# Kernel optimization log

Measured on AMD Instinct MI355X. Metric: run time of the kernel, lower is better.

## Reference

```python
import jax, jax.numpy as jnp
import numpy as np

N_NODES = 40000
N_EDGES = 640000
IN_DIM = 128
HID_DIM = 256
OUT_DIM = 256
N_CLASSES = 10
N_GRAPHS = 128
NEG_SLOPE = 0.01  # F.leaky_relu default


def setup_inputs() -> dict:
    key = jax.random.key(0)
    ks = jax.random.split(key, 10)
    x = jax.random.normal(ks[0], (N_NODES, IN_DIM), dtype=jnp.float32)
    src = jax.random.randint(ks[1], (N_EDGES,), 0, N_NODES, dtype=jnp.int64)
    dst = jax.random.randint(ks[2], (N_EDGES,), 0, N_NODES, dtype=jnp.int64)
    graph_ids = jnp.sort(jax.random.randint(ks[3], (N_NODES,), 0, N_GRAPHS, dtype=jnp.int64))
    # GraphConv weights (glorot-ish scale) and biases
    W1 = jax.random.normal(ks[4], (IN_DIM, HID_DIM), dtype=jnp.float32) * (1.0 / np.sqrt(IN_DIM))
    b1 = jnp.zeros((HID_DIM,), dtype=jnp.float32)
    W2 = jax.random.normal(ks[5], (HID_DIM, OUT_DIM), dtype=jnp.float32) * (1.0 / np.sqrt(HID_DIM))
    b2 = jnp.zeros((OUT_DIM,), dtype=jnp.float32)
    Wc = jax.random.normal(ks[6], (OUT_DIM, N_CLASSES), dtype=jnp.float32) * (1.0 / np.sqrt(OUT_DIM))
    bc = jnp.zeros((N_CLASSES,), dtype=jnp.float32)
    return {"x": x, "src": src, "dst": dst, "graph_ids": graph_ids,
            "W1": W1, "b1": b1, "W2": W2, "b2": b2, "Wc": Wc, "bc": bc}


def reference(x, src, dst, graph_ids, W1, b1, W2, b2, Wc, bc):
    n = x.shape[0]
    ones_e = jnp.ones((src.shape[0],), dtype=x.dtype)
    # degrees (clamped at 1, as DGL GraphConv does)
    outdeg = jnp.clip(jax.ops.segment_sum(ones_e, src, num_segments=n), 1.0)
    indeg = jnp.clip(jax.ops.segment_sum(ones_e, dst, num_segments=n), 1.0)
    inv_sqrt_out = jax.lax.rsqrt(outdeg)[:, None]   # [N,1]
    inv_sqrt_in = jax.lax.rsqrt(indeg)[:, None]     # [N,1]

    def gconv(h, W, b):
        # DGL GraphConv, norm='both': D_in^{-1/2} A D_out^{-1/2} h W + b
        m = h * inv_sqrt_out                                    # [N,d]
        agg = jnp.zeros((n, h.shape[1]), h.dtype).at[dst].add(m[src])
        agg = agg * inv_sqrt_in
        return agg @ W + b

    h = jax.nn.leaky_relu(gconv(x, W1, b1), negative_slope=NEG_SLOPE)
    h = jax.nn.leaky_relu(gconv(h, W2, b2), negative_slope=NEG_SLOPE)

    # dgl.mean_nodes: per-graph mean over nodes
    sums = jax.ops.segment_sum(h, graph_ids, num_segments=N_GRAPHS)        # [G,256]
    counts = jax.ops.segment_sum(jnp.ones((n,), h.dtype), graph_ids, num_segments=N_GRAPHS)
    hg = sums / jnp.clip(counts, 1.0)[:, None]
    return hg @ Wc + bc  # [G, n_classes]
```

## Files before the change

kernel.cpp:

```cpp
#include <hip/hip_runtime.h>

#define N_NODES 40000
#define N_EDGES 640000
#define IN_DIM 128
#define HID_DIM 256
#define OUT_DIM 256
#define N_CLASSES 10
#define N_GRAPHS 128
#define NEG_SLOPE 0.01f

#define SCAN_BLOCKS ((N_NODES + 255) / 256)

typedef short bf16x8 __attribute__((ext_vector_type(8)));
typedef float f32x4 __attribute__((ext_vector_type(4)));

__device__ inline unsigned short f2bf(float x) {
  unsigned u = __float_as_uint(x);
  u += 0x7fffu + ((u >> 16) & 1u);
  return (unsigned short)(u >> 16);
}
__device__ inline float bf2f(unsigned short h) {
  return __uint_as_float(((unsigned)h) << 16);
}
__device__ inline unsigned pack_split(float v) {
  unsigned short hi = f2bf(v);
  float r = v - bf2f(hi);
  unsigned short lo = f2bf(r);
  return (unsigned)hi | ((unsigned)lo << 16);
}

__global__ __launch_bounds__(256) void hist_kernel(const int* __restrict__ src,
                                                   const int* __restrict__ dst,
                                                   int* __restrict__ cntOut,
                                                   int* __restrict__ cntIn, int nEdges) {
  int i = blockIdx.x * 256 + threadIdx.x;
  if (i < nEdges) {
    atomicAdd(&cntOut[src[i]], 1);
    atomicAdd(&cntIn[dst[i]], 1);
  }
}

__global__ __launch_bounds__(256) void scan1_kernel(const int* __restrict__ cnt,
                                                    int* __restrict__ rowptr,
                                                    int* __restrict__ blockSums) {
  __shared__ int sm[256];
  int i = blockIdx.x * 256 + threadIdx.x;
  int v = (i < N_NODES) ? cnt[i] : 0;
  sm[threadIdx.x] = v;
  __syncthreads();
  for (int off = 1; off < 256; off <<= 1) {
    int t = (threadIdx.x >= off) ? sm[threadIdx.x - off] : 0;
    __syncthreads();
    sm[threadIdx.x] += t;
    __syncthreads();
  }
  if (i < N_NODES) rowptr[i] = sm[threadIdx.x] - v;
  if (threadIdx.x == 255) blockSums[blockIdx.x] = sm[255];
}

__global__ __launch_bounds__(256) void scan2_kernel(const int* __restrict__ blockSums,
                                                    int* __restrict__ blockOff,
                                                    int* __restrict__ rowptr) {
  __shared__ int sm[256];
  int tid = threadIdx.x;
  int v = (tid < SCAN_BLOCKS) ? blockSums[tid] : 0;
  sm[tid] = v;
  __syncthreads();
  for (int off = 1; off < 256; off <<= 1) {
    int t = (tid >= off) ? sm[tid - off] : 0;
    __syncthreads();
    sm[tid] += t;
    __syncthreads();
  }
  if (tid < SCAN_BLOCKS) blockOff[tid] = sm[tid] - v;
  if (tid == 255) rowptr[N_NODES] = sm[255];
}

__global__ __launch_bounds__(256) void scan3_kernel(int* __restrict__ rowptr,
                                                    const int* __restrict__ blockOff,
                                                    int* __restrict__ cursor,
                                                    const int* __restrict__ cntIn,
                                                    const int* __restrict__ cntOut,
                                                    float* __restrict__ sIn,
                                                    float* __restrict__ sOut,
                                                    float* __restrict__ poolZero, int nZero) {
  int i = blockIdx.x * 256 + threadIdx.x;
  if (i < N_NODES) {
    int r = rowptr[i] + blockOff[blockIdx.x];
    rowptr[i] = r;
    cursor[i] = r;
    sIn[i] = rsqrtf((float)max(cntIn[i], 1));
    sOut[i] = rsqrtf((float)max(cntOut[i], 1));
  }
  if (i < nZero) poolZero[i] = 0.0f;
}

__global__ __launch_bounds__(256) void fill_kernel(const int* __restrict__ src,
                                                   const int* __restrict__ dst,
                                                   int* __restrict__ cursor,
                                                   int* __restrict__ eidx, int nEdges) {
  int e = blockIdx.x * 256 + threadIdx.x;
  if (e < nEdges) {
    int pos = atomicAdd(&cursor[dst[e]], 1);
    eidx[pos] = src[e];
  }
}

__global__ __launch_bounds__(256) void wsplit_kernel(const float* __restrict__ W1,
                                                     unsigned* __restrict__ Wt1,
                                                     const float* __restrict__ W2,
                                                     unsigned* __restrict__ Wt2) {
  int i = blockIdx.x * 256 + threadIdx.x;
  constexpr int N1 = IN_DIM * 256;
  if (i < N1) {
    int k = i >> 8;
    int n = i & 255;
    Wt1[(size_t)n * IN_DIM + k] = pack_split(W1[i]);
  } else {
    int j = i - N1;
    if (j < HID_DIM * 256) {
      int k = j >> 8;
      int n = j & 255;
      Wt2[(size_t)n * HID_DIM + k] = pack_split(W2[j]);
    }
  }
}

template <int D, bool BF16>
__global__ __launch_bounds__(256) void gather_kernel(const void* __restrict__ hsrc,
                                                     const float* __restrict__ s_out,
                                                     const float* __restrict__ s_in,
                                                     const int* __restrict__ rowptr,
                                                     const int* __restrict__ eidx,
                                                     unsigned* __restrict__ aggp) {
  constexpr int VEC = D / 64;
  const int node = __builtin_amdgcn_readfirstlane(blockIdx.x * 4 + (threadIdx.x >> 6));
  const int lane = threadIdx.x & 63;
  const int f0 = lane * VEC;
  const int beg = rowptr[node];
  const int end = rowptr[node + 1];
  float acc[VEC] = {};
  int j = beg;
  for (; j + 7 < end; j += 8) {
    int s[8];
#pragma unroll
    for (int u = 0; u < 8; u++) s[u] = eidx[j + u];
    float v[8][VEC];
#pragma unroll
    for (int u = 0; u < 8; u++) {
      if constexpr (BF16) {
        const unsigned short* row = (const unsigned short*)hsrc + (size_t)s[u] * D + f0;
        if constexpr (VEC == 4) {
          uint2 rv = *reinterpret_cast<const uint2*>(row);
          v[u][0] = bf2f((unsigned short)(rv.x & 0xffffu));
          v[u][1] = bf2f((unsigned short)(rv.x >> 16));
          v[u][2] = bf2f((unsigned short)(rv.y & 0xffffu));
          v[u][3] = bf2f((unsigned short)(rv.y >> 16));
        } else {
          unsigned rv = *reinterpret_cast<const unsigned*>(row);
          v[u][0] = bf2f((unsigned short)(rv & 0xffffu));
          v[u][1] = bf2f((unsigned short)(rv >> 16));
        }
      } else {
        const float* row = (const float*)hsrc + (size_t)s[u] * D + f0;
        if constexpr (VEC == 4) {
          float4 t = *reinterpret_cast<const float4*>(row);
          v[u][0] = t.x; v[u][1] = t.y; v[u][2] = t.z; v[u][3] = t.w;
        } else {
          float2 t = *reinterpret_cast<const float2*>(row);
          v[u][0] = t.x; v[u][1] = t.y;
        }
      }
    }
    float c[8];
#pragma unroll
    for (int u = 0; u < 8; u++) c[u] = s_out[s[u]];
#pragma unroll
    for (int u = 0; u < 8; u++)
#pragma unroll
      for (int q = 0; q < VEC; q++) acc[q] += v[u][q] * c[u];
  }
  for (; j < end; j++) {
    int s = eidx[j];
    float c = s_out[s];
    if constexpr (BF16) {
      const unsigned short* row = (const unsigned short*)hsrc + (size_t)s * D + f0;
#pragma unroll
      for (int q = 0; q < VEC; q++) acc[q] += bf2f(row[q]) * c;
    } else {
      const float* row = (const float*)hsrc + (size_t)s * D + f0;
#pragma unroll
      for (int q = 0; q < VEC; q++) acc[q] += row[q] * c;
    }
  }
  float si = s_in[node];
#pragma unroll
  for (int q = 0; q < VEC; q++) aggp[(size_t)node * D + f0 + q] = pack_split(acc[q] * si);
}

template <int K, bool OUT_BF16>
__global__ __launch_bounds__(256) void gemm_mfma_bias_lrelu(const unsigned* __restrict__ Apk,
                                                            const unsigned* __restrict__ Wt,
                                                            const float* __restrict__ bias,
                                                            void* __restrict__ Optr, int M) {
  constexpr int BM = 128, BN = 128, BK = 32;
  constexpr int LDK = BK + 8;
  __shared__ unsigned short Ah[BM][LDK], Al[BM][LDK];
  __shared__ unsigned short Bh[BN][LDK], Bl[BN][LDK];
  const int tid = threadIdx.x;
  const int lane = tid & 63;
  const int wave = tid >> 6;
  const int wr = wave >> 1, wc = wave & 1;
  const int rowBase = blockIdx.x * BM;
  const int colBase = blockIdx.y * BN;
  const int g = lane >> 4;
  const int r16 = lane & 15;

  f32x4 acc[4][4] = {};

  for (int k0 = 0; k0 < K; k0 += BK) {
#pragma unroll
    for (int p = 0; p < 4; p++) {
      int e = (p * 256 + tid) * 4;
      int r = e >> 5;
      int kc = e & 31;
      int gr = rowBase + r;
      if (gr >= M) gr = M - 1;
      uint4 v = *reinterpret_cast<const uint4*>(&Apk[(size_t)gr * K + k0 + kc]);
      *reinterpret_cast<unsigned*>(&Ah[r][kc]) = (v.x & 0xffffu) | (v.y << 16);
      *reinterpret_cast<unsigned*>(&Ah[r][kc + 2]) = (v.z & 0xffffu) | (v.w << 16);
      *reinterpret_cast<unsigned*>(&Al[r][kc]) = (v.x >> 16) | (v.y & 0xffff0000u);
      *reinterpret_cast<unsigned*>(&Al[r][kc + 2]) = (v.z >> 16) | (v.w & 0xffff0000u);
    }
#pragma unroll
    for (int p = 0; p < 4; p++) {
      int e = (p * 256 + tid) * 4;
      int n = e >> 5;
      int kc = e & 31;
      uint4 v = *reinterpret_cast<const uint4*>(&Wt[(size_t)(colBase + n) * K + k0 + kc]);
      *reinterpret_cast<unsigned*>(&Bh[n][kc]) = (v.x & 0xffffu) | (v.y << 16);
      *reinterpret_cast<unsigned*>(&Bh[n][kc + 2]) = (v.z & 0xffffu) | (v.w << 16);
      *reinterpret_cast<unsigned*>(&Bl[n][kc]) = (v.x >> 16) | (v.y & 0xffff0000u);
      *reinterpret_cast<unsigned*>(&Bl[n][kc + 2]) = (v.z >> 16) | (v.w & 0xffff0000u);
    }
    __syncthreads();

    bf16x8 afh[4], afl[4], bfh[4], bfl[4];
#pragma unroll
    for (int mf = 0; mf < 4; mf++) {
      afh[mf] = *reinterpret_cast<const bf16x8*>(&Ah[wr * 64 + mf * 16 + r16][g * 8]);
      afl[mf] = *reinterpret_cast<const bf16x8*>(&Al[wr * 64 + mf * 16 + r16][g * 8]);
    }
#pragma unroll
    for (int nf = 0; nf < 4; nf++) {
      bfh[nf] = *reinterpret_cast<const bf16x8*>(&Bh[wc * 64 + nf * 16 + r16][g * 8]);
      bfl[nf] = *reinterpret_cast<const bf16x8*>(&Bl[wc * 64 + nf * 16 + r16][g * 8]);
    }
#pragma unroll
    for (int mf = 0; mf < 4; mf++)
#pragma unroll
      for (int nf = 0; nf < 4; nf++) {
        acc[mf][nf] = __builtin_amdgcn_mfma_f32_16x16x32_bf16(afh[mf], bfh[nf], acc[mf][nf], 0, 0, 0);
        acc[mf][nf] = __builtin_amdgcn_mfma_f32_16x16x32_bf16(afh[mf], bfl[nf], acc[mf][nf], 0, 0, 0);
        acc[mf][nf] = __builtin_amdgcn_mfma_f32_16x16x32_bf16(afl[mf], bfh[nf], acc[mf][nf], 0, 0, 0);
      }
    __syncthreads();
  }

#pragma unroll
  for (int mf = 0; mf < 4; mf++)
#pragma unroll
    for (int nf = 0; nf < 4; nf++) {
      int col = colBase + wc * 64 + nf * 16 + r16;
      float bv = bias[col];
#pragma unroll
      for (int j = 0; j < 4; j++) {
        int row = rowBase + wr * 64 + mf * 16 + g * 4 + j;
        if (row < M) {
          float v = acc[mf][nf][j] + bv;
          v = v > 0.0f ? v : NEG_SLOPE * v;
          if constexpr (OUT_BF16) {
            ((unsigned short*)Optr)[(size_t)row * 256 + col] = f2bf(v);
          } else {
            ((float*)Optr)[(size_t)row * 256 + col] = v;
          }
        }
      }
    }
}

__global__ __launch_bounds__(64) void pool_kernel(const float* __restrict__ h,
                                                  const int* __restrict__ gids,
                                                  float* __restrict__ sums,
                                                  float* __restrict__ counts, int nNodes) {
  constexpr int NB = 32;
  const int lane = threadIdx.x;
  const int n0 = blockIdx.x * NB;
  float4 acc = {0.0f, 0.0f, 0.0f, 0.0f};
  int cur = -1;
  int cnt = 0;
  for (int i = 0; i < NB; i++) {
    int n = n0 + i;
    if (n >= nNodes) break;
    int g = gids[n];
    if (g != cur) {
      if (cur >= 0) {
        float* sp = &sums[(size_t)cur * 256 + lane * 4];
        atomicAdd(sp + 0, acc.x);
        atomicAdd(sp + 1, acc.y);
        atomicAdd(sp + 2, acc.z);
        atomicAdd(sp + 3, acc.w);
        if (lane == 0) atomicAdd(&counts[cur], (float)cnt);
      }
      cur = g;
      acc = {0.0f, 0.0f, 0.0f, 0.0f};
      cnt = 0;
    }
    float4 v = *reinterpret_cast<const float4*>(&h[(size_t)n * 256 + lane * 4]);
    acc.x += v.x;
    acc.y += v.y;
    acc.z += v.z;
    acc.w += v.w;
    cnt++;
  }
  if (cur >= 0) {
    float* sp = &sums[(size_t)cur * 256 + lane * 4];
    atomicAdd(sp + 0, acc.x);
    atomicAdd(sp + 1, acc.y);
    atomicAdd(sp + 2, acc.z);
    atomicAdd(sp + 3, acc.w);
    if (lane == 0) atomicAdd(&counts[cur], (float)cnt);
  }
}

__global__ __launch_bounds__(256) void cls_kernel(const float* __restrict__ sums,
                                                  const float* __restrict__ counts,
                                                  const float* __restrict__ Wc,
                                                  const float* __restrict__ bc,
                                                  float* __restrict__ out) {
  __shared__ float hg[256];
  int g = blockIdx.x;
  float invc = 1.0f / fmaxf(counts[g], 1.0f);
  hg[threadIdx.x] = sums[(size_t)g * 256 + threadIdx.x] * invc;
  __syncthreads();
  if (threadIdx.x < N_CLASSES) {
    float a = bc[threadIdx.x];
    for (int k = 0; k < 256; k++) a += hg[k] * Wc[k * N_CLASSES + threadIdx.x];
    out[g * N_CLASSES + threadIdx.x] = a;
  }
}

static constexpr size_t align1k(size_t x) { return (x + 1023) & ~(size_t)1023; }

extern "C" void kernel_launch(void* const* d_in, const int* in_sizes, int n_in,
                              void* d_out, int out_size, void* d_ws, size_t ws_size,
                              hipStream_t stream) {
  const float* x = (const float*)d_in[0];
  const int* src = (const int*)d_in[1];
  const int* dst = (const int*)d_in[2];
  const int* gids = (const int*)d_in[3];
  const float* W1 = (const float*)d_in[4];
  const float* b1 = (const float*)d_in[5];
  const float* W2 = (const float*)d_in[6];
  const float* b2 = (const float*)d_in[7];
  const float* Wc = (const float*)d_in[8];
  const float* bc = (const float*)d_in[9];
  float* out = (float*)d_out;

  char* ws = (char*)d_ws;
  constexpr size_t OFF_CNT_IN = 0;
  constexpr size_t OFF_CNT_OUT = OFF_CNT_IN + (size_t)N_NODES * 4;
  constexpr size_t OFF_ROWPTR = align1k(OFF_CNT_OUT + (size_t)N_NODES * 4);
  constexpr size_t OFF_CURSOR = align1k(OFF_ROWPTR + (size_t)(N_NODES + 1) * 4);
  constexpr size_t OFF_BSUM = align1k(OFF_CURSOR + (size_t)N_NODES * 4);
  constexpr size_t OFF_BOFF = align1k(OFF_BSUM + 1024);
  constexpr size_t OFF_SIN = align1k(OFF_BOFF + 1024);
  constexpr size_t OFF_SOUT = OFF_SIN + (size_t)N_NODES * 4;
  constexpr size_t OFF_PCNT = align1k(OFF_SOUT + (size_t)N_NODES * 4);
  constexpr size_t OFF_SUMS = align1k(OFF_PCNT + 512);
  constexpr size_t OFF_EIDX = align1k(OFF_SUMS + (size_t)N_GRAPHS * 256 * 4);
  constexpr size_t OFF_AGG = align1k(OFF_EIDX + (size_t)N_EDGES * 4);
  constexpr size_t SZ_BIG = (size_t)N_NODES * 256 * 4;
  constexpr size_t OFF_H = align1k(OFF_AGG + SZ_BIG);
  constexpr size_t OFF_WT1 = align1k(OFF_H + SZ_BIG);
  constexpr size_t OFF_WT2 = align1k(OFF_WT1 + 256 * 128 * 4);

  int* cntIn = (int*)(ws + OFF_CNT_IN);
  int* cntOut = (int*)(ws + OFF_CNT_OUT);
  int* rowptr = (int*)(ws + OFF_ROWPTR);
  int* cursor = (int*)(ws + OFF_CURSOR);
  int* bsum = (int*)(ws + OFF_BSUM);
  int* boff = (int*)(ws + OFF_BOFF);
  float* s_in = (float*)(ws + OFF_SIN);
  float* s_out = (float*)(ws + OFF_SOUT);
  float* counts = (float*)(ws + OFF_PCNT);
  float* sums = (float*)(ws + OFF_SUMS);
  int* eidx = (int*)(ws + OFF_EIDX);
  unsigned* aggp = (unsigned*)(ws + OFF_AGG);
  unsigned short* h1b = (unsigned short*)(ws + OFF_H);
  float* h2 = (float*)(ws + OFF_H);
  unsigned* Wt1 = (unsigned*)(ws + OFF_WT1);
  unsigned* Wt2 = (unsigned*)(ws + OFF_WT2);

  hipMemsetAsync(ws + OFF_CNT_IN, 0, 2 * (size_t)N_NODES * 4, stream);

  const int nZero = (int)((OFF_SUMS - OFF_PCNT) / 4 + (size_t)N_GRAPHS * 256);

  hist_kernel<<<(N_EDGES + 255) / 256, 256, 0, stream>>>(src, dst, cntOut, cntIn, N_EDGES);
  scan1_kernel<<<SCAN_BLOCKS, 256, 0, stream>>>(cntIn, rowptr, bsum);
  scan2_kernel<<<1, 256, 0, stream>>>(bsum, boff, rowptr);
  scan3_kernel<<<SCAN_BLOCKS, 256, 0, stream>>>(rowptr, boff, cursor, cntIn, cntOut, s_in, s_out,
                                                counts, nZero);
  fill_kernel<<<(N_EDGES + 255) / 256, 256, 0, stream>>>(src, dst, cursor, eidx, N_EDGES);
  wsplit_kernel<<<((IN_DIM + HID_DIM) * 256 + 255) / 256, 256, 0, stream>>>(W1, Wt1, W2, Wt2);

  dim3 ggrid((N_NODES + 127) / 128, 2);

  gather_kernel<IN_DIM, false><<<N_NODES / 4, 256, 0, stream>>>(x, s_out, s_in, rowptr, eidx, aggp);
  gemm_mfma_bias_lrelu<IN_DIM, true><<<ggrid, 256, 0, stream>>>(aggp, Wt1, b1, h1b, N_NODES);

  gather_kernel<HID_DIM, true><<<N_NODES / 4, 256, 0, stream>>>(h1b, s_out, s_in, rowptr, eidx, aggp);
  gemm_mfma_bias_lrelu<HID_DIM, false><<<ggrid, 256, 0, stream>>>(aggp, Wt2, b2, h2, N_NODES);

  pool_kernel<<<(N_NODES + 31) / 32, 64, 0, stream>>>(h2, gids, sums, counts, N_NODES);
  cls_kernel<<<N_GRAPHS, 256, 0, stream>>>(sums, counts, Wc, bc, out);
}
```

Measured before the change: 361.4 us.

## Use LDS-sliced degree histograms and gather layer-1 features from fp16 copy

Measured after the change: 340.6 us. -5.8%, faster.

```diff
diff --git a/kernel.cpp b/kernel.cpp
--- a/kernel.cpp
+++ b/kernel.cpp
@@ -10,6 +10,7 @@
 #define NEG_SLOPE 0.01f
 
 #define SCAN_BLOCKS ((N_NODES + 255) / 256)
+#define NSLICE 16
 
 typedef short bf16x8 __attribute__((ext_vector_type(8)));
 typedef float f32x4 __attribute__((ext_vector_type(4)));
@@ -28,24 +29,64 @@
   unsigned short lo = f2bf(r);
   return (unsigned)hi | ((unsigned)lo << 16);
 }
-
-__global__ __launch_bounds__(256) void hist_kernel(const int* __restrict__ src,
-                                                   const int* __restrict__ dst,
-                                                   int* __restrict__ cntOut,
-                                                   int* __restrict__ cntIn, int nEdges) {
-  int i = blockIdx.x * 256 + threadIdx.x;
-  if (i < nEdges) {
-    atomicAdd(&cntOut[src[i]], 1);
-    atomicAdd(&cntIn[dst[i]], 1);
-  }
-}
-
-__global__ __launch_bounds__(256) void scan1_kernel(const int* __restrict__ cnt,
+__device__ inline float h2f(unsigned short u) {
+  _Float16 h;
+  __builtin_memcpy(&h, &u, 2);
+  return (float)h;
+}
+__device__ inline unsigned short f2h(float x) {
+  _Float16 h = (_Float16)x;
+  unsigned short u;
+  __builtin_memcpy(&u, &h, 2);
+  return u;
+}
+
+__global__ __launch_bounds__(256) void hist_lds_kernel(const int* __restrict__ dst,
+                                                       const int* __restrict__ src,
+                                                       int* __restrict__ partials) {
+  __shared__ int hbin[N_NODES];
+  const int slice = blockIdx.x;
+  const int dir = blockIdx.y;
+  const int* keys = dir ? src : dst;
+  for (int i = threadIdx.x; i < N_NODES; i += 256) hbin[i] = 0;
+  __syncthreads();
+  constexpr int PER = N_EDGES / NSLICE;
+  const int e0 = slice * PER;
+  for (int e = e0 + threadIdx.x; e < e0 + PER; e += 256) atomicAdd(&hbin[keys[e]], 1);
+  __syncthreads();
+  int* out = partials + ((size_t)dir * NSLICE + slice) * N_NODES;
+  for (int i = threadIdx.x; i < N_NODES; i += 256) out[i] = hbin[i];
+}
+
+__global__ __launch_bounds__(256) void xhalf_kernel(const float* __restrict__ x,
+                                                    unsigned short* __restrict__ xh) {
+  int base = (blockIdx.x * 256 + threadIdx.x) * 8;
+  if (base < N_NODES * IN_DIM) {
+    float4 a = *reinterpret_cast<const float4*>(&x[base]);
+    float4 b = *reinterpret_cast<const float4*>(&x[base + 4]);
+    unsigned short o[8];
+    const float* pa = &a.x;
+    const float* pb = &b.x;
+#pragma unroll
+    for (int q = 0; q < 4; q++) o[q] = f2h(pa[q]);
+#pragma unroll
+    for (int q = 0; q < 4; q++) o[4 + q] = f2h(pb[q]);
+    *reinterpret_cast<uint4*>(&xh[base]) = *reinterpret_cast<const uint4*>(o);
+  }
+}
+
+__global__ __launch_bounds__(256) void scan1_kernel(const int* __restrict__ partials,
+                                                    int* __restrict__ cntIn,
                                                     int* __restrict__ rowptr,
                                                     int* __restrict__ blockSums) {
   __shared__ int sm[256];
   int i = blockIdx.x * 256 + threadIdx.x;
-  int v = (i < N_NODES) ? cnt[i] : 0;
+  int v = 0;
+  if (i < N_NODES) {
+#pragma unroll
+    for (int s = 0; s < NSLICE; s++) v += partials[(size_t)s * N_NODES + i];
+    cntIn[i] = v;
+  }
   sm[threadIdx.x] = v;
   __syncthreads();
   for (int off = 1; off < 256; off <<= 1) {
@@ -80,7 +121,7 @@
                                                     const int* __restrict__ blockOff,
                                                     int* __restrict__ cursor,
                                                     const int* __restrict__ cntIn,
-                                                    const int* __restrict__ cntOut,
+                                                    const int* __restrict__ part1,
                                                     float* __restrict__ sIn,
                                                     float* __restrict__ sOut,
                                                     float* __restrict__ poolZero, int nZero) {
@@ -90,7 +131,10 @@
     rowptr[i] = r;
     cursor[i] = r;
     sIn[i] = rsqrtf((float)max(cntIn[i], 1));
-    sOut[i] = rsqrtf((float)max(cntOut[i], 1));
+    int co = 0;
+#pragma unroll
+    for (int s = 0; s < NSLICE; s++) co += part1[(size_t)s * N_NODES + i];
+    sOut[i] = rsqrtf((float)max(co, 1));
   }
   if (i < nZero) poolZero[i] = 0.0f;
 }
@@ -126,7 +170,7 @@
   }
 }
 
-template <int D, bool BF16>
+template <int D, int MODE>
 __global__ __launch_bounds__(256) void gather_kernel(const void* __restrict__ hsrc,
                                                      const float* __restrict__ s_out,
                                                      const float* __restrict__ s_in,
@@ -148,20 +192,7 @@
     float v[8][VEC];
 #pragma unroll
     for (int u = 0; u < 8; u++) {
-      if constexpr (BF16) {
-        const unsigned short* row = (const unsigned short*)hsrc + (size_t)s[u] * D + f0;
-        if constexpr (VEC == 4) {
-          uint2 rv = *reinterpret_cast<const uint2*>(row);
-          v[u][0] = bf2f((unsigned short)(rv.x & 0xffffu));
-          v[u][1] = bf2f((unsigned short)(rv.x >> 16));
-          v[u][2] = bf2f((unsigned short)(rv.y & 0xffffu));
-          v[u][3] = bf2f((unsigned short)(rv.y >> 16));
-        } else {
-          unsigned rv = *reinterpret_cast<const unsigned*>(row);
-          v[u][0] = bf2f((unsigned short)(rv & 0xffffu));
-          v[u][1] = bf2f((unsigned short)(rv >> 16));
-        }
-      } else {
+      if constexpr (MODE == 0) {
         const float* row = (const float*)hsrc + (size_t)s[u] * D + f0;
         if constexpr (VEC == 4) {
           float4 t = *reinterpret_cast<const float4*>(row);
@@ -170,6 +201,20 @@
           float2 t = *reinterpret_cast<const float2*>(row);
           v[u][0] = t.x; v[u][1] = t.y;
         }
+      } else {
+        const unsigned short* row = (const unsigned short*)hsrc + (size_t)s[u] * D + f0;
+        if constexpr (VEC == 4) {
+          uint2 rv = *reinterpret_cast<const uint2*>(row);
+          unsigned short w[4] = {(unsigned short)(rv.x & 0xffffu), (unsigned short)(rv.x >> 16),
+                                 (unsigned short)(rv.y & 0xffffu), (unsigned short)(rv.y >> 16)};
+#pragma unroll
+          for (int q = 0; q < 4; q++) v[u][q] = (MODE == 1) ? bf2f(w[q]) : h2f(w[q]);
+        } else {
+          unsigned rv = *reinterpret_cast<const unsigned*>(row);
+          unsigned short w[2] = {(unsigned short)(rv & 0xffffu), (unsigned short)(rv >> 16)};
+#pragma unroll
+          for (int q = 0; q < 2; q++) v[u][q] = (MODE == 1) ? bf2f(w[q]) : h2f(w[q]);
+        }
       }
     }
     float c[8];
@@ -183,14 +228,15 @@
   for (; j < end; j++) {
     int s = eidx[j];
     float c = s_out[s];
-    if constexpr (BF16) {
+    if constexpr (MODE == 0) {
+      const float* row = (const float*)hsrc + (size_t)s * D + f0;
+#pragma unroll
+      for (int q = 0; q < VEC; q++) acc[q] += row[q] * c;
+    } else {
       const unsigned short* row = (const unsigned short*)hsrc + (size_t)s * D + f0;
 #pragma unroll
-      for (int q = 0; q < VEC; q++) acc[q] += bf2f(row[q]) * c;
-    } else {
-      const float* row = (const float*)hsrc + (size_t)s * D + f0;
-#pragma unroll
-      for (int q = 0; q < VEC; q++) acc[q] += row[q] * c;
+      for (int q = 0; q < VEC; q++)
+        acc[q] += ((MODE == 1) ? bf2f(row[q]) : h2f(row[q])) * c;
     }
   }
   float si = s_in[node];
@@ -369,8 +415,7 @@
 
   char* ws = (char*)d_ws;
   constexpr size_t OFF_CNT_IN = 0;
-  constexpr size_t OFF_CNT_OUT = OFF_CNT_IN + (size_t)N_NODES * 4;
-  constexpr size_t OFF_ROWPTR = align1k(OFF_CNT_OUT + (size_t)N_NODES * 4);
+  constexpr size_t OFF_ROWPTR = align1k(OFF_CNT_IN + (size_t)N_NODES * 4);
   constexpr size_t OFF_CURSOR = align1k(OFF_ROWPTR + (size_t)(N_NODES + 1) * 4);
   constexpr size_t OFF_BSUM = align1k(OFF_CURSOR + (size_t)N_NODES * 4);
   constexpr size_t OFF_BOFF = align1k(OFF_BSUM + 1024);
@@ -384,9 +429,10 @@
   constexpr size_t OFF_H = align1k(OFF_AGG + SZ_BIG);
   constexpr size_t OFF_WT1 = align1k(OFF_H + SZ_BIG);
   constexpr size_t OFF_WT2 = align1k(OFF_WT1 + 256 * 128 * 4);
+  constexpr size_t OFF_PART = align1k(OFF_WT2 + 256 * 256 * 4);
+  constexpr size_t OFF_XH = align1k(OFF_PART + (size_t)2 * NSLICE * N_NODES * 4);
 
   int* cntIn = (int*)(ws + OFF_CNT_IN);
-  int* cntOut = (int*)(ws + OFF_CNT_OUT);
   int* rowptr = (int*)(ws + OFF_ROWPTR);
   int* cursor = (int*)(ws + OFF_CURSOR);
   int* bsum = (int*)(ws + OFF_BSUM);
@@ -401,25 +447,27 @@
   float* h2 = (float*)(ws + OFF_H);
   unsigned* Wt1 = (unsigned*)(ws + OFF_WT1);
   unsigned* Wt2 = (unsigned*)(ws + OFF_WT2);
-
-  hipMemsetAsync(ws + OFF_CNT_IN, 0, 2 * (size_t)N_NODES * 4, stream);
+  int* partials = (int*)(ws + OFF_PART);
+  unsigned short* xh = (unsigned short*)(ws + OFF_XH);
 
   const int nZero = (int)((OFF_SUMS - OFF_PCNT) / 4 + (size_t)N_GRAPHS * 256);
 
-  hist_kernel<<<(N_EDGES + 255) / 256, 256, 0, stream>>>(src, dst, cntOut, cntIn, N_EDGES);
-  scan1_kernel<<<SCAN_BLOCKS, 256, 0, stream>>>(cntIn, rowptr, bsum);
+  hist_lds_kernel<<<dim3(NSLICE, 2), 256, 0, stream>>>(dst, src, partials);
+  xhalf_kernel<<<(N_NODES * IN_DIM / 8 + 255) / 256, 256, 0, stream>>>(x, xh);
+  wsplit_kernel<<<((IN_DIM + HID_DIM) * 256 + 255) / 256, 256, 0, stream>>>(W1, Wt1, W2, Wt2);
+  scan1_kernel<<<SCAN_BLOCKS, 256, 0, stream>>>(partials, cntIn, rowptr, bsum);
   scan2_kernel<<<1, 256, 0, stream>>>(bsum, boff, rowptr);
-  scan3_kernel<<<SCAN_BLOCKS, 256, 0, stream>>>(rowptr, boff, cursor, cntIn, cntOut, s_in, s_out,
+  scan3_kernel<<<SCAN_BLOCKS, 256, 0, stream>>>(rowptr, boff, cursor, cntIn,
+                                                partials + (size_t)NSLICE * N_NODES, s_in, s_out,
                                                 counts, nZero);
   fill_kernel<<<(N_EDGES + 255) / 256, 256, 0, stream>>>(src, dst, cursor, eidx, N_EDGES);
-  wsplit_kernel<<<((IN_DIM + HID_DIM) * 256 + 255) / 256, 256, 0, stream>>>(W1, Wt1, W2, Wt2);
 
   dim3 ggrid((N_NODES + 127) / 128, 2);
 
-  gather_kernel<IN_DIM, false><<<N_NODES / 4, 256, 0, stream>>>(x, s_out, s_in, rowptr, eidx, aggp);
+  gather_kernel<IN_DIM, 2><<<N_NODES / 4, 256, 0, stream>>>(xh, s_out, s_in, rowptr, eidx, aggp);
   gemm_mfma_bias_lrelu<IN_DIM, true><<<ggrid, 256, 0, stream>>>(aggp, Wt1, b1, h1b, N_NODES);
 
-  gather_kernel<HID_DIM, true><<<N_NODES / 4, 256, 0, stream>>>(h1b, s_out, s_in, rowptr, eidx, aggp);
+  gather_kernel<HID_DIM, 1><<<N_NODES / 4, 256, 0, stream>>>(h1b, s_out, s_in, rowptr, eidx, aggp);
   gemm_mfma_bias_lrelu<HID_DIM, false><<<ggrid, 256, 0, stream>>>(aggp, Wt2, b2, h2, N_NODES);
 
   pool_kernel<<<(N_NODES + 31) / 32, 64, 0, stream>>>(h2, gids, sums, counts, N_NODES);
```
